# Kernel tuning notes

Measured on AMD Instinct MI355X. Metric: run time of the kernel, lower is better.

Reference implementation:

```python
import jax, jax.numpy as jnp
import numpy as np

K = 16          # max neighbors per ball query
RADIUS = 1.0    # ball radius
SEQ_LEN = 4
N_POINTS = 8192


def ball_query_idx(xyz, radius, k):
    """PointNet++-style ball query of xyz against itself.
    xyz: [N, 3]. Returns [N, k] int32: the first k in-radius source indices
    (in ascending index order, matching the CUDA kernel's scan order),
    padded with the first in-radius index when fewer than k are found.
    Self-distance is 0 < radius so every row has at least one hit.
    """
    n = xyz.shape[0]
    # squared pairwise distances via the matmul expansion: ||a-b||^2 = ||a||^2 + ||b||^2 - 2 a.b
    sq = jnp.sum(xyz * xyz, axis=-1)                          # [N]
    d2 = sq[:, None] + sq[None, :] - 2.0 * (xyz @ xyz.T)      # [N, N]
    cand = jnp.where(d2 < radius * radius, jnp.arange(n, dtype=jnp.int32)[None, :], n)
    firstk = jnp.sort(cand, axis=-1)[:, :k]                   # first k hits in index order, n = no-hit sentinel
    first = firstk[:, :1]                                     # first in-radius index (always valid)
    return jnp.where(firstk == n, first, firstk)              # pad missing slots with first hit


def setup_inputs() -> dict:
    key = jax.random.key(0)
    k1, k2 = jax.random.split(key)
    pc_source = jax.random.normal(k1, (1, N_POINTS, 3), dtype=jnp.float32)
    pred_flow = jax.random.normal(k2, (SEQ_LEN, N_POINTS, 3), dtype=jnp.float32)
    return {"pc_source": pc_source, "pred_flow": pred_flow}


def reference(pc_source, pred_flow):
    # idx from pc_source (batch 1), broadcast across the sequence (idx.repeat in torch)
    idx = ball_query_idx(pc_source[0], RADIUS, K)             # [N, k]
    flow = jnp.transpose(pred_flow, (0, 2, 1))                # [S, 3, N]
    nn_flow = flow[:, :, idx]                                 # grouping_operation -> [S, 3, N, k]
    diff = flow[..., None] - nn_flow                          # [S, 3, N, k]
    # p=2 norm over the channel dim (safe sqrt: self-neighbor diff is exactly 0)
    dist = jnp.sqrt(jnp.maximum(jnp.sum(diff * diff, axis=1), 1e-24))  # [S, N, k]
    # .mean(dim=-1) over k, then .mean(dim=-1) over N (no weights branch), then .mean() over S
    return dist.mean(axis=-1).mean(axis=-1).mean()
```

## Files before the change

### kernel.cpp

```cpp
#include <hip/hip_runtime.h>
#include <math.h>

#define NP 8192
#define SEQ 4
#define KNN 16
#define R2 1.0f
#define NBLK (NP / 4)
#define SCALE (1.0f / (float)(SEQ * NP * KNN))
#define POISON 0xAAAAAAAAu

__global__ __launch_bounds__(256) void ballq_fused(
    const float* __restrict__ xyz,
    const float* __restrict__ pf,
    float* __restrict__ partial,
    float* __restrict__ out)
{
    const int lane = threadIdx.x & 63;
    const int wv   = threadIdx.x >> 6;

    if (blockIdx.x == NBLK) {
        float v[8];
        unsigned done = 0;
        const unsigned* up = (const unsigned*)partial;
        while (done != 0xFFu) {
#pragma unroll
            for (int r = 0; r < 8; ++r) {
                if (!(done & (1u << r))) {
                    const unsigned u = __hip_atomic_load(
                        &up[(r << 8) + threadIdx.x],
                        __ATOMIC_RELAXED, __HIP_MEMORY_SCOPE_AGENT);
                    if (u != POISON) { v[r] = __uint_as_float(u); done |= 1u << r; }
                }
            }
        }
        float s = 0.0f;
#pragma unroll
        for (int r = 0; r < 8; ++r) s += v[r];
#pragma unroll
        for (int off = 32; off > 0; off >>= 1) s += __shfl_xor(s, off);
        __shared__ float w[4];
        if (lane == 0) w[wv] = s;
        __syncthreads();
        if (threadIdx.x == 0)
            out[0] = (w[0] + w[1] + w[2] + w[3]) * SCALE;
        return;
    }

    const int i = (blockIdx.x << 2) + wv;

    const float xi = xyz[3 * i + 0];
    const float yi = xyz[3 * i + 1];
    const float zi = xyz[3 * i + 2];

    const int s = lane >> 4;
    const size_t oi = ((size_t)s * NP + i) * 3;
    const float pix = pf[oi + 0];
    const float piy = pf[oi + 1];
    const float piz = pf[oi + 2];

    __shared__ int slots[4][KNN];
    int cnt = 0;

    for (int base = 0; base < NP; base += 1024) {
        float fx[16], fy[16], fz[16];
#pragma unroll
        for (int u = 0; u < 16; ++u) {
            const int j = base + (u << 6) + lane;
            fx[u] = xyz[3 * j + 0];
            fy[u] = xyz[3 * j + 1];
            fz[u] = xyz[3 * j + 2];
        }
#pragma unroll
        for (int u = 0; u < 16; ++u) {
            const float dx = fx[u] - xi;
            const float dy = fy[u] - yi;
            const float dz = fz[u] - zi;
            const bool hit = dx * dx + dy * dy + dz * dz < R2;
            const unsigned long long m = __ballot(hit);
            if (hit) {
                const int rank = __builtin_amdgcn_mbcnt_hi(
                    (unsigned)(m >> 32),
                    __builtin_amdgcn_mbcnt_lo((unsigned)m, 0));
                const int g = cnt + rank;
                if (g < KNN) slots[wv][g] = base + (u << 6) + lane;
            }
            cnt += __popcll(m);
        }
        if (cnt >= KNN) break;
    }

    int si = lane & 15;
    if (si >= cnt) si = 0;
    const int j = slots[wv][si];

    const size_t oj = ((size_t)s * NP + j) * 3;
    const float dx = pix - pf[oj + 0];
    const float dy = piy - pf[oj + 1];
    const float dz = piz - pf[oj + 2];
    float d = sqrtf(fmaxf(dx * dx + dy * dy + dz * dz, 1e-24f));

#pragma unroll
    for (int off = 32; off > 0; off >>= 1) d += __shfl_xor(d, off);

    __shared__ float sacc[4];
    if (lane == 0) sacc[wv] = d;
    __syncthreads();
    if (threadIdx.x == 0) {
        const float p = sacc[0] + sacc[1] + sacc[2] + sacc[3];
        __hip_atomic_store(&partial[blockIdx.x], p,
                           __ATOMIC_RELAXED, __HIP_MEMORY_SCOPE_AGENT);
    }
}

extern "C" void kernel_launch(void* const* d_in, const int* in_sizes, int n_in,
                              void* d_out, int out_size, void* d_ws, size_t ws_size,
                              hipStream_t stream) {
    const float* xyz = (const float*)d_in[0];
    const float* pf  = (const float*)d_in[1];
    float* partial   = (float*)d_ws;
    float* out       = (float*)d_out;

    ballq_fused<<<NBLK + 1, 256, 0, stream>>>(xyz, pf, partial, out);
}
```

Before: 68.13 us.

## Stage candidate point window in shared memory with block-wide early exit

Each 1024-point window of xyz is now loaded cooperatively into LDS once per block with float4 loads, instead of every wavefront loading it separately from global memory into registers. A shared done flag plus two barriers per window lets the block stop once all four waves have found their neighbors. Launch bounds now request 8 blocks per SM so register pressure drops. The trade-off is block-wide synchronisation: a wave that is already done must wait for the slowest wave, and the LDS reads are strided by 3 floats, which may cause bank conflicts.

Measured after the change: 74.07 us. 8.7% more time.

```diff
diff --git a/kernel.cpp b/kernel.cpp
--- a/kernel.cpp
+++ b/kernel.cpp
@@ -6,10 +6,11 @@
 #define KNN 16
 #define R2 1.0f
 #define NBLK (NP / 4)
+#define WIN 1024
 #define SCALE (1.0f / (float)(SEQ * NP * KNN))
 #define POISON 0xAAAAAAAAu
 
-__global__ __launch_bounds__(256) void ballq_fused(
+__global__ __launch_bounds__(256, 8) void ballq_fused(
     const float* __restrict__ xyz,
     const float* __restrict__ pf,
     float* __restrict__ partial,
@@ -58,35 +59,43 @@
     const float piy = pf[oi + 1];
     const float piz = pf[oi + 2];
 
+    __shared__ float4 win4[(WIN * 3) / 4];
     __shared__ int slots[4][KNN];
+    __shared__ int sdone;
+    const float* win = (const float*)win4;
+
     int cnt = 0;
 
-    for (int base = 0; base < NP; base += 1024) {
-        float fx[16], fy[16], fz[16];
+    for (int base = 0; base < NP; base += WIN) {
+        const float4* src = (const float4*)(xyz + 3 * base);
 #pragma unroll
-        for (int u = 0; u < 16; ++u) {
-            const int j = base + (u << 6) + lane;
-            fx[u] = xyz[3 * j + 0];
-            fy[u] = xyz[3 * j + 1];
-            fz[u] = xyz[3 * j + 2];
+        for (int t = 0; t < 3; ++t)
+            win4[(t << 8) + threadIdx.x] = src[(t << 8) + threadIdx.x];
+        if (threadIdx.x == 0) sdone = 1;
+        __syncthreads();
+
+        if (cnt < KNN) {
+#pragma unroll
+            for (int u = 0; u < 16; ++u) {
+                const int jl = (u << 6) + lane;
+                const float dx = win[3 * jl + 0] - xi;
+                const float dy = win[3 * jl + 1] - yi;
+                const float dz = win[3 * jl + 2] - zi;
+                const bool hit = dx * dx + dy * dy + dz * dz < R2;
+                const unsigned long long m = __ballot(hit);
+                if (hit) {
+                    const int rank = __builtin_amdgcn_mbcnt_hi(
+                        (unsigned)(m >> 32),
+                        __builtin_amdgcn_mbcnt_lo((unsigned)m, 0));
+                    const int g = cnt + rank;
+                    if (g < KNN) slots[wv][g] = base + jl;
+                }
+                cnt += __popcll(m);
+            }
+            if (cnt < KNN && lane == 0) sdone = 0;
         }
-#pragma unroll
-        for (int u = 0; u < 16; ++u) {
-            const float dx = fx[u] - xi;
-            const float dy = fy[u] - yi;
-            const float dz = fz[u] - zi;
-            const bool hit = dx * dx + dy * dy + dz * dz < R2;
-            const unsigned long long m = __ballot(hit);
-            if (hit) {
-                const int rank = __builtin_amdgcn_mbcnt_hi(
-                    (unsigned)(m >> 32),
-                    __builtin_amdgcn_mbcnt_lo((unsigned)m, 0));
-                const int g = cnt + rank;
-                if (g < KNN) slots[wv][g] = base + (u << 6) + lane;
-            }
-            cnt += __popcll(m);
-        }
-        if (cnt >= KNN) break;
+        __syncthreads();
+        if (sdone) break;
     }
 
     int si = lane & 15;
```

## Scan candidates in 256-point windows with float4 loads and prefetch

Applied to the files above, without the earlier changes.

The ball-query scan changes from 1024-point chunks of scalar strided loads to 256-point windows. Each lane loads four consecutive points as three float4 vectors, and the next window is prefetched while the current one is processed. Hit ranks are computed from four ballots, using an interleaved per-lane order so the ascending index order is kept. The smaller window lets a wave stop earlier once 16 hits are found, which cuts wasted loads. Launch bounds also request higher occupancy. The cost is one extra prefetch load that wraps around at the end of the point set.

After: 69.65 us. 2.2% more time.

```diff
diff --git a/kernel.cpp b/kernel.cpp
--- a/kernel.cpp
+++ b/kernel.cpp
@@ -6,10 +6,16 @@
 #define KNN 16
 #define R2 1.0f
 #define NBLK (NP / 4)
+#define WIN 256
 #define SCALE (1.0f / (float)(SEQ * NP * KNN))
 #define POISON 0xAAAAAAAAu
 
-__global__ __launch_bounds__(256) void ballq_fused(
+__device__ __forceinline__ int mbcnt64(unsigned long long m) {
+    return __builtin_amdgcn_mbcnt_hi((unsigned)(m >> 32),
+           __builtin_amdgcn_mbcnt_lo((unsigned)m, 0));
+}
+
+__global__ __launch_bounds__(256, 4) void ballq_fused(
     const float* __restrict__ xyz,
     const float* __restrict__ pf,
     float* __restrict__ partial,
@@ -59,34 +65,50 @@
     const float piz = pf[oi + 2];
 
     __shared__ int slots[4][KNN];
+    const float4* F = (const float4*)xyz;
+
     int cnt = 0;
 
-    for (int base = 0; base < NP; base += 1024) {
-        float fx[16], fy[16], fz[16];
-#pragma unroll
-        for (int u = 0; u < 16; ++u) {
-            const int j = base + (u << 6) + lane;
-            fx[u] = xyz[3 * j + 0];
-            fy[u] = xyz[3 * j + 1];
-            fz[u] = xyz[3 * j + 2];
-        }
-#pragma unroll
-        for (int u = 0; u < 16; ++u) {
-            const float dx = fx[u] - xi;
-            const float dy = fy[u] - yi;
-            const float dz = fz[u] - zi;
-            const bool hit = dx * dx + dy * dy + dz * dz < R2;
-            const unsigned long long m = __ballot(hit);
-            if (hit) {
-                const int rank = __builtin_amdgcn_mbcnt_hi(
-                    (unsigned)(m >> 32),
-                    __builtin_amdgcn_mbcnt_lo((unsigned)m, 0));
-                const int g = cnt + rank;
-                if (g < KNN) slots[wv][g] = base + (u << 6) + lane;
-            }
-            cnt += __popcll(m);
-        }
+    float4 A = F[3 * lane + 0];
+    float4 B = F[3 * lane + 1];
+    float4 C = F[3 * lane + 2];
+
+    for (int base = 0; base < NP; base += WIN) {
+        const int nf = ((3 * ((base + WIN) & (NP - 1))) >> 2) + 3 * lane;
+        const float4 A2 = F[nf + 0];
+        const float4 B2 = F[nf + 1];
+        const float4 C2 = F[nf + 2];
+
+        const float dx0 = A.x - xi, dy0 = A.y - yi, dz0 = A.z - zi;
+        const float dx1 = A.w - xi, dy1 = B.x - yi, dz1 = B.y - zi;
+        const float dx2 = B.z - xi, dy2 = B.w - yi, dz2 = C.x - zi;
+        const float dx3 = C.y - xi, dy3 = C.z - yi, dz3 = C.w - zi;
+        const bool h0 = dx0 * dx0 + dy0 * dy0 + dz0 * dz0 < R2;
+        const bool h1 = dx1 * dx1 + dy1 * dy1 + dz1 * dz1 < R2;
+        const bool h2 = dx2 * dx2 + dy2 * dy2 + dz2 * dz2 < R2;
+        const bool h3 = dx3 * dx3 + dy3 * dy3 + dz3 * dz3 < R2;
+        const unsigned long long m0 = __ballot(h0);
+        const unsigned long long m1 = __ballot(h1);
+        const unsigned long long m2 = __ballot(h2);
+        const unsigned long long m3 = __ballot(h3);
+
+        const int pre = mbcnt64(m0) + mbcnt64(m1) + mbcnt64(m2) + mbcnt64(m3);
+        const int o0 = (int)((m0 >> lane) & 1ull);
+        const int o1 = (int)((m1 >> lane) & 1ull);
+        const int o2 = (int)((m2 >> lane) & 1ull);
+        const int g0 = cnt + pre;
+        const int g1 = g0 + o0;
+        const int g2 = g1 + o1;
+        const int g3 = g2 + o2;
+        const int c0 = base + 4 * lane;
+        if (h0 && g0 < KNN) slots[wv][g0] = c0 + 0;
+        if (h1 && g1 < KNN) slots[wv][g1] = c0 + 1;
+        if (h2 && g2 < KNN) slots[wv][g2] = c0 + 2;
+        if (h3 && g3 < KNN) slots[wv][g3] = c0 + 3;
+
+        cnt += __popcll(m0) + __popcll(m1) + __popcll(m2) + __popcll(m3);
         if (cnt >= KNN) break;
+        A = A2; B = B2; C = C2;
     }
 
     int si = lane & 15;
```
